# Performance work log

Measured on AMD Instinct MI355X. Metric: run time of the kernel, lower is better.

## Reference

```python
import jax, jax.numpy as jnp
import numpy as np

N, F_IN, F_OUT, C = 4096, 512, 256, 4


def setup_inputs() -> dict:
    key = jax.random.key(0)
    k1, k2, k3, k4 = jax.random.split(key, 4)
    stdv = 1.0 / np.sqrt(F_OUT)
    x = jax.random.normal(k1, (N, F_IN), dtype=jnp.float32)
    adjs = jax.random.normal(k2, (N, N, C), dtype=jnp.float32)
    weight = jax.random.uniform(k3, (F_IN, F_OUT, C), dtype=jnp.float32, minval=-stdv, maxval=stdv)
    bias = jax.random.uniform(k4, (N, F_OUT, C), dtype=jnp.float32, minval=-stdv, maxval=stdv)
    return {"x": x, "adjs": adjs, "weight": weight, "bias": bias}


def _fft_product(X, Y):
    # t-product: FFT along channel axis, per-frequency matmul, IFFT, real part
    Xf = jnp.fft.fft(X, axis=-1)
    Yf = jnp.fft.fft(Y, axis=-1)
    Zf = jnp.einsum('ijk,jrk->irk', Xf, Yf)
    return jnp.fft.ifft(Zf, axis=-1).real.astype(X.dtype)


def reference(x, adjs, weight, bias):
    C_ = adjs.shape[-1]
    # x.repeat(C,1,1).permute(1,2,0) -> [N, F, C]
    x3 = jnp.broadcast_to(x[:, :, None], (x.shape[0], x.shape[1], C_))
    h = _fft_product(x3, weight)      # [N, F_OUT, C]
    out = _fft_product(adjs, h)       # [N, F_OUT, C]
    return out + bias
```

## Files before the change

### kernel.cpp

```cpp
#include <hip/hip_runtime.h>
#include <cstdint>
#include <cstddef>

#define NN   4096
#define FIN  512
#define FOUT 256

typedef short bf16x8 __attribute__((ext_vector_type(8)));
typedef float f32x4  __attribute__((ext_vector_type(4)));

__device__ __forceinline__ unsigned short f2bf(float f) {
    union { float f; unsigned u; } v; v.f = f;
    unsigned r = v.u + 0x7FFFu + ((v.u >> 16) & 1u);
    return (unsigned short)(r >> 16);
}

__global__ __launch_bounds__(256) void k_prep_wsum(const float4* __restrict__ w4,
                                                   unsigned short* __restrict__ wsumT) {
    int t = blockIdx.x * 256 + threadIdx.x;
    int r = t & (FOUT - 1);
    int j = t >> 8;
    float4 v = w4[j * FOUT + r];
    wsumT[r * FIN + j] = f2bf(v.x + v.y + v.z + v.w);
}

template<int K, int MODE>
__global__ __launch_bounds__(512) void k_gemm16(
    const void* __restrict__ Aptr,
    const unsigned short* __restrict__ Bt,
    unsigned short* __restrict__ Ht,
    const float4* __restrict__ bias4,
    float4* __restrict__ out4)
{
    constexpr int NCHUNK = K / 64;
    __shared__ unsigned short Abf[16 * 72];

    const int tid  = threadIdx.x;
    const int lane = tid & 63;
    const int wave = tid >> 6;
    const int quad = lane >> 4;
    const int l15  = lane & 15;
    const int i0   = blockIdx.x * 16;

    const int si = tid >> 5;
    const int sk = (tid & 31) * 2;

    f32x4 acc0 = {0.f, 0.f, 0.f, 0.f};
    f32x4 acc1 = {0.f, 0.f, 0.f, 0.f};

    float4 pa0, pa1;
    bf16x8 bp00, bp01, bp10, bp11;

    auto loadA = [&](int c) {
        const int j0 = c * 64;
        if (MODE == 0) {
            const float* xp = (const float*)Aptr;
            const float2 t2 = *(const float2*)(xp + (size_t)(i0 + si) * FIN + j0 + sk);
            pa0.x = t2.x; pa0.y = t2.y;
        } else {
            const float4* ap = (const float4*)Aptr;
            size_t base = (size_t)(i0 + si) * NN + j0 + sk;
            pa0 = ap[base];
            pa1 = ap[base + 1];
        }
    };
    auto loadB = [&](int c, bf16x8& b00, bf16x8& b01, bf16x8& b10, bf16x8& b11) {
        const int j0 = c * 64;
        const unsigned short* p0 = Bt + (size_t)(wave * 32 + l15) * K + j0 + quad * 8;
        b00 = *(const bf16x8*)(p0);
        b01 = *(const bf16x8*)(p0 + 32);
        const unsigned short* p1 = p0 + (size_t)16 * K;
        b10 = *(const bf16x8*)(p1);
        b11 = *(const bf16x8*)(p1 + 32);
    };

    loadA(0);
    loadB(0, bp00, bp01, bp10, bp11);

    for (int c = 0; c < NCHUNK; ++c) {
        __syncthreads();
        if (MODE == 0) {
            unsigned pack = (unsigned)f2bf(pa0.x) | ((unsigned)f2bf(pa0.y) << 16);
            *(unsigned*)&Abf[si * 72 + sk] = pack;
        } else {
            float s0 = (pa0.x + pa0.y) + (pa0.z + pa0.w);
            float s1 = (pa1.x + pa1.y) + (pa1.z + pa1.w);
            *(unsigned*)&Abf[si * 72 + sk] =
                (unsigned)f2bf(s0) | ((unsigned)f2bf(s1) << 16);
        }
        __syncthreads();

        bf16x8 bc00 = bp00, bc01 = bp01, bc10 = bp10, bc11 = bp11;
        if (c + 1 < NCHUNK) {
            loadA(c + 1);
            loadB(c + 1, bp00, bp01, bp10, bp11);
        }

        bf16x8 a0 = *(const bf16x8*)&Abf[l15 * 72 + quad * 8];
        bf16x8 a1 = *(const bf16x8*)&Abf[l15 * 72 + 32 + quad * 8];

        acc0 = __builtin_amdgcn_mfma_f32_16x16x32_bf16(a0, bc00, acc0, 0, 0, 0);
        acc0 = __builtin_amdgcn_mfma_f32_16x16x32_bf16(a1, bc01, acc0, 0, 0, 0);
        acc1 = __builtin_amdgcn_mfma_f32_16x16x32_bf16(a0, bc10, acc1, 0, 0, 0);
        acc1 = __builtin_amdgcn_mfma_f32_16x16x32_bf16(a1, bc11, acc1, 0, 0, 0);
    }

    if (MODE == 0) {
        const int n  = wave * 32 + l15;
        const int ib = i0 + quad * 4;
        ushort4 h;
        h.x = f2bf(acc0[0]); h.y = f2bf(acc0[1]); h.z = f2bf(acc0[2]); h.w = f2bf(acc0[3]);
        *(ushort4*)(Ht + (size_t)n * NN + ib) = h;
        h.x = f2bf(acc1[0]); h.y = f2bf(acc1[1]); h.z = f2bf(acc1[2]); h.w = f2bf(acc1[3]);
        *(ushort4*)(Ht + (size_t)(n + 16) * NN + ib) = h;
    } else {
        const int col = wave * 32 + l15;
        const int ib  = i0 + quad * 4;
#pragma unroll
        for (int r = 0; r < 4; ++r) {
            size_t idx = (size_t)(ib + r) * FOUT + col;
            float4 bv = bias4[idx];
            float  s  = acc0[r];
            float4 o; o.x = s + bv.x; o.y = s + bv.y; o.z = s + bv.z; o.w = s + bv.w;
            out4[idx] = o;
            float4 bv1 = bias4[idx + 16];
            float  s1  = acc1[r];
            float4 o1; o1.x = s1 + bv1.x; o1.y = s1 + bv1.y; o1.z = s1 + bv1.z; o1.w = s1 + bv1.w;
            out4[idx + 16] = o1;
        }
    }
}

extern "C" void kernel_launch(void* const* d_in, const int* in_sizes, int n_in,
                              void* d_out, int out_size, void* d_ws, size_t ws_size,
                              hipStream_t stream) {
    const float*  x     = (const float*)d_in[0];
    const float4* adjs4 = (const float4*)d_in[1];
    const float4* w4    = (const float4*)d_in[2];
    const float4* bias4 = (const float4*)d_in[3];
    float4*       out4  = (float4*)d_out;

    unsigned short* wsumT = (unsigned short*)d_ws;
    unsigned short* Ht    = (unsigned short*)((char*)d_ws + (size_t)FOUT * FIN * 2);

    k_prep_wsum<<<(FIN * FOUT) / 256, 256, 0, stream>>>(w4, wsumT);
    k_gemm16<FIN, 0><<<NN / 16, 512, 0, stream>>>((const void*)x, wsumT, Ht, nullptr, nullptr);
    k_gemm16<NN, 1><<<NN / 16, 512, 0, stream>>>((const void*)adjs4, Ht, nullptr, bias4, out4);
}
```

Before: 397.9 us.

## Widen K chunks to 256 with double-buffered LDS and deeper prefetch

Raises the K step from 64 to 256 and double-buffers the A tile in LDS, prefetching two chunks ahead in registers so more memory loads are in flight per barrier. The adjacency stream, bias reads and output writes become nontemporal loads and stores. The aim is to hide latency in the bandwidth-bound adjs GEMM and to halve barrier overhead per unit of work. It costs many more registers (A and B prefetch arrays) and sets launch bounds to 2 blocks per CU, which may cause register spilling.

```diff
diff --git a/kernel.cpp b/kernel.cpp
--- a/kernel.cpp
+++ b/kernel.cpp
@@ -5,35 +5,41 @@
 #define NN   4096
 #define FIN  512
 #define FOUT 256
+#define BK   256
+#define LDSK 264
 
 typedef short bf16x8 __attribute__((ext_vector_type(8)));
 typedef float f32x4  __attribute__((ext_vector_type(4)));
+typedef float f32x2  __attribute__((ext_vector_type(2)));
 
 __device__ __forceinline__ unsigned short f2bf(float f) {
     union { float f; unsigned u; } v; v.f = f;
     unsigned r = v.u + 0x7FFFu + ((v.u >> 16) & 1u);
     return (unsigned short)(r >> 16);
 }
+__device__ __forceinline__ unsigned pack2(float a, float b) {
+    return (unsigned)f2bf(a) | ((unsigned)f2bf(b) << 16);
+}
 
-__global__ __launch_bounds__(256) void k_prep_wsum(const float4* __restrict__ w4,
+__global__ __launch_bounds__(256) void k_prep_wsum(const f32x4* __restrict__ w4,
                                                    unsigned short* __restrict__ wsumT) {
     int t = blockIdx.x * 256 + threadIdx.x;
     int r = t & (FOUT - 1);
     int j = t >> 8;
-    float4 v = w4[j * FOUT + r];
-    wsumT[r * FIN + j] = f2bf(v.x + v.y + v.z + v.w);
+    f32x4 v = w4[j * FOUT + r];
+    wsumT[r * FIN + j] = f2bf((v.x + v.y) + (v.z + v.w));
 }
 
 template<int K, int MODE>
-__global__ __launch_bounds__(512) void k_gemm16(
+__global__ __launch_bounds__(512, 2) void k_gemm16(
     const void* __restrict__ Aptr,
     const unsigned short* __restrict__ Bt,
     unsigned short* __restrict__ Ht,
-    const float4* __restrict__ bias4,
-    float4* __restrict__ out4)
+    const f32x4* __restrict__ bias4,
+    f32x4* __restrict__ out4)
 {
-    constexpr int NCHUNK = K / 64;
-    __shared__ unsigned short Abf[16 * 72];
+    constexpr int NCHUNK = K / BK;
+    __shared__ unsigned short Abf[2][16 * LDSK];
 
     const int tid  = threadIdx.x;
     const int lane = tid & 63;
@@ -42,67 +48,80 @@
     const int l15  = lane & 15;
     const int i0   = blockIdx.x * 16;
 
-    const int si = tid >> 5;
-    const int sk = (tid & 31) * 2;
+    const int si  = tid >> 5;
+    const int c32 = tid & 31;
 
     f32x4 acc0 = {0.f, 0.f, 0.f, 0.f};
     f32x4 acc1 = {0.f, 0.f, 0.f, 0.f};
 
-    float4 pa0, pa1;
-    bf16x8 bp00, bp01, bp10, bp11;
-
-    auto loadA = [&](int c) {
-        const int j0 = c * 64;
+    auto loadA = [&](int c, f32x4* pa, f32x2* pf) {
+        const int kb = c * BK;
         if (MODE == 0) {
-            const float* xp = (const float*)Aptr;
-            const float2 t2 = *(const float2*)(xp + (size_t)(i0 + si) * FIN + j0 + sk);
-            pa0.x = t2.x; pa0.y = t2.y;
+            const float* xp = (const float*)Aptr + (size_t)(i0 + si) * FIN + kb + c32 * 2;
+#pragma unroll
+            for (int u = 0; u < 4; ++u)
+                pf[u] = __builtin_nontemporal_load((const f32x2*)(xp + u * 64));
         } else {
-            const float4* ap = (const float4*)Aptr;
-            size_t base = (size_t)(i0 + si) * NN + j0 + sk;
-            pa0 = ap[base];
-            pa1 = ap[base + 1];
+            const f32x4* ap = (const f32x4*)Aptr + (size_t)(i0 + si) * NN + kb + c32 * 2;
+#pragma unroll
+            for (int u = 0; u < 4; ++u) {
+                pa[2 * u]     = __builtin_nontemporal_load(ap + u * 64);
+                pa[2 * u + 1] = __builtin_nontemporal_load(ap + u * 64 + 1);
+            }
         }
     };
-    auto loadB = [&](int c, bf16x8& b00, bf16x8& b01, bf16x8& b10, bf16x8& b11) {
-        const int j0 = c * 64;
-        const unsigned short* p0 = Bt + (size_t)(wave * 32 + l15) * K + j0 + quad * 8;
-        b00 = *(const bf16x8*)(p0);
-        b01 = *(const bf16x8*)(p0 + 32);
-        const unsigned short* p1 = p0 + (size_t)16 * K;
-        b10 = *(const bf16x8*)(p1);
-        b11 = *(const bf16x8*)(p1 + 32);
+    auto writeA = [&](int b, const f32x4* pa, const f32x2* pf) {
+        unsigned* dst = (unsigned*)&Abf[b][si * LDSK + c32 * 2];
+        if (MODE == 0) {
+#pragma unroll
+            for (int u = 0; u < 4; ++u)
+                dst[u * 32] = pack2(pf[u].x, pf[u].y);
+        } else {
+#pragma unroll
+            for (int u = 0; u < 4; ++u) {
+                f32x4 p0 = pa[2 * u], p1 = pa[2 * u + 1];
+                dst[u * 32] = pack2((p0.x + p0.y) + (p0.z + p0.w),
+                                    (p1.x + p1.y) + (p1.z + p1.w));
+            }
+        }
+    };
+    auto loadB = [&](int c, bf16x8* b0, bf16x8* b1) {
+        const unsigned short* p0 = Bt + (size_t)(wave * 32 + l15) * K + c * BK + quad * 8;
+#pragma unroll
+        for (int s = 0; s < 8; ++s) {
+            b0[s] = *(const bf16x8*)(p0 + s * 32);
+            b1[s] = *(const bf16x8*)(p0 + (size_t)16 * K + s * 32);
+        }
+    };
+    auto compute = [&](int b, const bf16x8* b0, const bf16x8* b1) {
+        const unsigned short* arow = &Abf[b][l15 * LDSK + quad * 8];
+#pragma unroll
+        for (int s = 0; s < 8; ++s) {
+            bf16x8 a = *(const bf16x8*)(arow + s * 32);
+            acc0 = __builtin_amdgcn_mfma_f32_16x16x32_bf16(a, b0[s], acc0, 0, 0, 0);
+            acc1 = __builtin_amdgcn_mfma_f32_16x16x32_bf16(a, b1[s], acc1, 0, 0, 0);
+        }
     };
 
-    loadA(0);
-    loadB(0, bp00, bp01, bp10, bp11);
+    f32x4 paX[8], paY[8];
+    f32x2 pfX[4], pfY[4];
+    bf16x8 b0X[8], b1X[8], b0Y[8], b1Y[8];
 
-    for (int c = 0; c < NCHUNK; ++c) {
+    loadA(0, paX, pfX); loadB(0, b0X, b1X);
+    loadA(1, paY, pfY); loadB(1, b0Y, b1Y);
+
+    for (int c = 0; c < NCHUNK; c += 2) {
+        writeA(0, paX, pfX);
+        { int cn = (c + 2 < NCHUNK) ? c + 2 : 0; loadA(cn, paX, pfX); }
         __syncthreads();
-        if (MODE == 0) {
-            unsigned pack = (unsigned)f2bf(pa0.x) | ((unsigned)f2bf(pa0.y) << 16);
-            *(unsigned*)&Abf[si * 72 + sk] = pack;
-        } else {
-            float s0 = (pa0.x + pa0.y) + (pa0.z + pa0.w);
-            float s1 = (pa1.x + pa1.y) + (pa1.z + pa1.w);
-            *(unsigned*)&Abf[si * 72 + sk] =
-                (unsigned)f2bf(s0) | ((unsigned)f2bf(s1) << 16);
-        }
+        compute(0, b0X, b1X);
+        { int cn = (c + 2 < NCHUNK) ? c + 2 : 0; loadB(cn, b0X, b1X); }
+
+        writeA(1, paY, pfY);
+        { int cn = (c + 3 < NCHUNK) ? c + 3 : 1; loadA(cn, paY, pfY); }
         __syncthreads();
-
-        bf16x8 bc00 = bp00, bc01 = bp01, bc10 = bp10, bc11 = bp11;
-        if (c + 1 < NCHUNK) {
-            loadA(c + 1);
-            loadB(c + 1, bp00, bp01, bp10, bp11);
-        }
-
-        bf16x8 a0 = *(const bf16x8*)&Abf[l15 * 72 + quad * 8];
-        bf16x8 a1 = *(const bf16x8*)&Abf[l15 * 72 + 32 + quad * 8];
-
-        acc0 = __builtin_amdgcn_mfma_f32_16x16x32_bf16(a0, bc00, acc0, 0, 0, 0);
-        acc0 = __builtin_amdgcn_mfma_f32_16x16x32_bf16(a1, bc01, acc0, 0, 0, 0);
-        acc1 = __builtin_amdgcn_mfma_f32_16x16x32_bf16(a0, bc10, acc1, 0, 0, 0);
-        acc1 = __builtin_amdgcn_mfma_f32_16x16x32_bf16(a1, bc11, acc1, 0, 0, 0);
+        compute(1, b0Y, b1Y);
+        { int cn = (c + 3 < NCHUNK) ? c + 3 : 1; loadB(cn, b0Y, b1Y); }
     }
 
     if (MODE == 0) {
@@ -119,14 +138,14 @@
 #pragma unroll
         for (int r = 0; r < 4; ++r) {
             size_t idx = (size_t)(ib + r) * FOUT + col;
-            float4 bv = bias4[idx];
-            float  s  = acc0[r];
-            float4 o; o.x = s + bv.x; o.y = s + bv.y; o.z = s + bv.z; o.w = s + bv.w;
-            out4[idx] = o;
-            float4 bv1 = bias4[idx + 16];
-            float  s1  = acc1[r];
-            float4 o1; o1.x = s1 + bv1.x; o1.y = s1 + bv1.y; o1.z = s1 + bv1.z; o1.w = s1 + bv1.w;
-            out4[idx + 16] = o1;
+            f32x4 bv = __builtin_nontemporal_load(bias4 + idx);
+            float s  = acc0[r];
+            f32x4 o; o.x = s + bv.x; o.y = s + bv.y; o.z = s + bv.z; o.w = s + bv.w;
+            __builtin_nontemporal_store(o, out4 + idx);
+            f32x4 bv1 = __builtin_nontemporal_load(bias4 + idx + 16);
+            float s1  = acc1[r];
+            f32x4 o1; o1.x = s1 + bv1.x; o1.y = s1 + bv1.y; o1.z = s1 + bv1.z; o1.w = s1 + bv1.w;
+            __builtin_nontemporal_store(o1, out4 + idx + 16);
         }
     }
 }
@@ -134,16 +153,16 @@
 extern "C" void kernel_launch(void* const* d_in, const int* in_sizes, int n_in,
                               void* d_out, int out_size, void* d_ws, size_t ws_size,
                               hipStream_t stream) {
-    const float*  x     = (const float*)d_in[0];
-    const float4* adjs4 = (const float4*)d_in[1];
-    const float4* w4    = (const float4*)d_in[2];
-    const float4* bias4 = (const float4*)d_in[3];
-    float4*       out4  = (float4*)d_out;
+    const float* x     = (const float*)d_in[0];
+    const void*  adjs  = d_in[1];
+    const f32x4* w4    = (const f32x4*)d_in[2];
+    const f32x4* bias4 = (const f32x4*)d_in[3];
+    f32x4*       out4  = (f32x4*)d_out;
 
     unsigned short* wsumT = (unsigned short*)d_ws;
     unsigned short* Ht    = (unsigned short*)((char*)d_ws + (size_t)FOUT * FIN * 2);
 
     k_prep_wsum<<<(FIN * FOUT) / 256, 256, 0, stream>>>(w4, wsumT);
     k_gemm16<FIN, 0><<<NN / 16, 512, 0, stream>>>((const void*)x, wsumT, Ht, nullptr, nullptr);
-    k_gemm16<NN, 1><<<NN / 16, 512, 0, stream>>>((const void*)adjs4, Ht, nullptr, bias4, out4);
+    k_gemm16<NN, 1><<<NN / 16, 512, 0, stream>>>(adjs, Ht, nullptr, bias4, out4);
 }
```

New measurement: 420.2 us. 1.06x slower.

## Split-K big GEMM with 64-row tiles, double-buffered LDS, and reduce kernel

Applied to the files above, without the earlier changes.

The adjacency GEMM moves to a dedicated kernel. Each block now computes a 64-row tile over a quarter of K, so one B fragment feeds four row sub-tiles and the Ht fragments are reused more. The A tile is double-buffered in LDS and read with nontemporal loads. Partial sums go to a workspace and a new reduce kernel adds them with the bias, which costs about 16MB of extra partial-sum traffic and one more launch.

```diff
diff --git a/kernel.cpp b/kernel.cpp
--- a/kernel.cpp
+++ b/kernel.cpp
@@ -8,68 +8,53 @@
 
 typedef short bf16x8 __attribute__((ext_vector_type(8)));
 typedef float f32x4  __attribute__((ext_vector_type(4)));
+typedef float f32x2  __attribute__((ext_vector_type(2)));
 
 __device__ __forceinline__ unsigned short f2bf(float f) {
     union { float f; unsigned u; } v; v.f = f;
     unsigned r = v.u + 0x7FFFu + ((v.u >> 16) & 1u);
     return (unsigned short)(r >> 16);
 }
-
-__global__ __launch_bounds__(256) void k_prep_wsum(const float4* __restrict__ w4,
+__device__ __forceinline__ unsigned pack2(float a, float b) {
+    return (unsigned)f2bf(a) | ((unsigned)f2bf(b) << 16);
+}
+
+__global__ __launch_bounds__(256) void k_prep_wsum(const f32x4* __restrict__ w4,
                                                    unsigned short* __restrict__ wsumT) {
     int t = blockIdx.x * 256 + threadIdx.x;
     int r = t & (FOUT - 1);
     int j = t >> 8;
-    float4 v = w4[j * FOUT + r];
-    wsumT[r * FIN + j] = f2bf(v.x + v.y + v.z + v.w);
-}
-
-template<int K, int MODE>
-__global__ __launch_bounds__(512) void k_gemm16(
-    const void* __restrict__ Aptr,
-    const unsigned short* __restrict__ Bt,
-    unsigned short* __restrict__ Ht,
-    const float4* __restrict__ bias4,
-    float4* __restrict__ out4)
-{
-    constexpr int NCHUNK = K / 64;
+    f32x4 v = w4[j * FOUT + r];
+    wsumT[r * FIN + j] = f2bf((v.x + v.y) + (v.z + v.w));
+}
+
+__global__ __launch_bounds__(512) void k_gemm_h(const float* __restrict__ x,
+                                                const unsigned short* __restrict__ Bt,
+                                                unsigned short* __restrict__ Ht) {
     __shared__ unsigned short Abf[16 * 72];
-
     const int tid  = threadIdx.x;
     const int lane = tid & 63;
     const int wave = tid >> 6;
     const int quad = lane >> 4;
     const int l15  = lane & 15;
     const int i0   = blockIdx.x * 16;
-
-    const int si = tid >> 5;
-    const int sk = (tid & 31) * 2;
+    const int si   = tid >> 5;
+    const int sk   = (tid & 31) * 2;
 
     f32x4 acc0 = {0.f, 0.f, 0.f, 0.f};
     f32x4 acc1 = {0.f, 0.f, 0.f, 0.f};
 
-    float4 pa0, pa1;
+    f32x2 pf;
     bf16x8 bp00, bp01, bp10, bp11;
 
     auto loadA = [&](int c) {
-        const int j0 = c * 64;
-        if (MODE == 0) {
-            const float* xp = (const float*)Aptr;
-            const float2 t2 = *(const float2*)(xp + (size_t)(i0 + si) * FIN + j0 + sk);
-            pa0.x = t2.x; pa0.y = t2.y;
-        } else {
-            const float4* ap = (const float4*)Aptr;
-            size_t base = (size_t)(i0 + si) * NN + j0 + sk;
-            pa0 = ap[base];
-            pa1 = ap[base + 1];
-        }
+        pf = *(const f32x2*)(x + (size_t)(i0 + si) * FIN + c * 64 + sk);
     };
     auto loadB = [&](int c, bf16x8& b00, bf16x8& b01, bf16x8& b10, bf16x8& b11) {
-        const int j0 = c * 64;
-        const unsigned short* p0 = Bt + (size_t)(wave * 32 + l15) * K + j0 + quad * 8;
+        const unsigned short* p0 = Bt + (size_t)(wave * 32 + l15) * FIN + c * 64 + quad * 8;
         b00 = *(const bf16x8*)(p0);
         b01 = *(const bf16x8*)(p0 + 32);
-        const unsigned short* p1 = p0 + (size_t)16 * K;
+        const unsigned short* p1 = p0 + (size_t)16 * FIN;
         b10 = *(const bf16x8*)(p1);
         b11 = *(const bf16x8*)(p1 + 32);
     };
@@ -77,25 +62,16 @@
     loadA(0);
     loadB(0, bp00, bp01, bp10, bp11);
 
-    for (int c = 0; c < NCHUNK; ++c) {
-        __syncthreads();
-        if (MODE == 0) {
-            unsigned pack = (unsigned)f2bf(pa0.x) | ((unsigned)f2bf(pa0.y) << 16);
-            *(unsigned*)&Abf[si * 72 + sk] = pack;
-        } else {
-            float s0 = (pa0.x + pa0.y) + (pa0.z + pa0.w);
-            float s1 = (pa1.x + pa1.y) + (pa1.z + pa1.w);
-            *(unsigned*)&Abf[si * 72 + sk] =
-                (unsigned)f2bf(s0) | ((unsigned)f2bf(s1) << 16);
-        }
+    for (int c = 0; c < FIN / 64; ++c) {
+        __syncthreads();
+        *(unsigned*)&Abf[si * 72 + sk] = pack2(pf.x, pf.y);
         __syncthreads();
 
         bf16x8 bc00 = bp00, bc01 = bp01, bc10 = bp10, bc11 = bp11;
-        if (c + 1 < NCHUNK) {
+        if (c + 1 < FIN / 64) {
             loadA(c + 1);
             loadB(c + 1, bp00, bp01, bp10, bp11);
         }
-
         bf16x8 a0 = *(const bf16x8*)&Abf[l15 * 72 + quad * 8];
         bf16x8 a1 = *(const bf16x8*)&Abf[l15 * 72 + 32 + quad * 8];
 
@@ -105,45 +81,139 @@
         acc1 = __builtin_amdgcn_mfma_f32_16x16x32_bf16(a1, bc11, acc1, 0, 0, 0);
     }
 
-    if (MODE == 0) {
-        const int n  = wave * 32 + l15;
-        const int ib = i0 + quad * 4;
-        ushort4 h;
-        h.x = f2bf(acc0[0]); h.y = f2bf(acc0[1]); h.z = f2bf(acc0[2]); h.w = f2bf(acc0[3]);
-        *(ushort4*)(Ht + (size_t)n * NN + ib) = h;
-        h.x = f2bf(acc1[0]); h.y = f2bf(acc1[1]); h.z = f2bf(acc1[2]); h.w = f2bf(acc1[3]);
-        *(ushort4*)(Ht + (size_t)(n + 16) * NN + ib) = h;
-    } else {
-        const int col = wave * 32 + l15;
-        const int ib  = i0 + quad * 4;
-#pragma unroll
-        for (int r = 0; r < 4; ++r) {
-            size_t idx = (size_t)(ib + r) * FOUT + col;
-            float4 bv = bias4[idx];
-            float  s  = acc0[r];
-            float4 o; o.x = s + bv.x; o.y = s + bv.y; o.z = s + bv.z; o.w = s + bv.w;
-            out4[idx] = o;
-            float4 bv1 = bias4[idx + 16];
-            float  s1  = acc1[r];
-            float4 o1; o1.x = s1 + bv1.x; o1.y = s1 + bv1.y; o1.z = s1 + bv1.z; o1.w = s1 + bv1.w;
-            out4[idx + 16] = o1;
-        }
+    const int n  = wave * 32 + l15;
+    const int ib = i0 + quad * 4;
+    ushort4 h;
+    h.x = f2bf(acc0[0]); h.y = f2bf(acc0[1]); h.z = f2bf(acc0[2]); h.w = f2bf(acc0[3]);
+    *(ushort4*)(Ht + (size_t)n * NN + ib) = h;
+    h.x = f2bf(acc1[0]); h.y = f2bf(acc1[1]); h.z = f2bf(acc1[2]); h.w = f2bf(acc1[3]);
+    *(ushort4*)(Ht + (size_t)(n + 16) * NN + ib) = h;
+}
+
+#define LD 72
+__global__ __launch_bounds__(512) void k_gemm_big(const f32x4* __restrict__ adjs4,
+                                                  const unsigned short* __restrict__ Bt,
+                                                  float* __restrict__ P) {
+    __shared__ unsigned short Abf[2][64 * LD];
+
+    const int tid  = threadIdx.x;
+    const int lane = tid & 63;
+    const int wave = tid >> 6;
+    const int quad = lane >> 4;
+    const int l15  = lane & 15;
+
+    const int kq   = blockIdx.x & 3;
+    const int rg   = blockIdx.x >> 2;
+    const int row0 = rg * 64;
+    const size_t kbase = (size_t)kq * 1024;
+
+    const int sr = tid >> 3;
+    const int sc = tid & 7;
+
+    f32x4 acc[4][2];
+#pragma unroll
+    for (int m = 0; m < 4; ++m)
+#pragma unroll
+        for (int n = 0; n < 2; ++n)
+            acc[m][n] = (f32x4){0.f, 0.f, 0.f, 0.f};
+
+    f32x4 pa[8];
+    bf16x8 pb[2][2];
+
+    auto loadA = [&](int c) {
+        const f32x4* ap = adjs4 + (size_t)(row0 + sr) * NN + kbase + c * 64;
+#pragma unroll
+        for (int u = 0; u < 4; ++u) {
+            pa[2 * u]     = __builtin_nontemporal_load(ap + sc * 2 + u * 16);
+            pa[2 * u + 1] = __builtin_nontemporal_load(ap + sc * 2 + u * 16 + 1);
+        }
+    };
+    auto writeA = [&](int b) {
+        unsigned* dst = (unsigned*)&Abf[b][sr * LD + sc * 2];
+#pragma unroll
+        for (int u = 0; u < 4; ++u) {
+            f32x4 p0 = pa[2 * u], p1 = pa[2 * u + 1];
+            dst[u * 8] = pack2((p0.x + p0.y) + (p0.z + p0.w),
+                               (p1.x + p1.y) + (p1.z + p1.w));
+        }
+    };
+    auto loadB = [&](int c) {
+#pragma unroll
+        for (int n = 0; n < 2; ++n) {
+            const unsigned short* p = Bt + (size_t)(wave * 32 + n * 16 + l15) * NN
+                                        + kbase + c * 64 + quad * 8;
+            pb[n][0] = *(const bf16x8*)p;
+            pb[n][1] = *(const bf16x8*)(p + 32);
+        }
+    };
+
+    loadA(0);
+    loadB(0);
+
+    for (int c = 0; c < 16; ++c) {
+        const int b = c & 1;
+        writeA(b);
+        if (c + 1 < 16) loadA(c + 1);
+        __syncthreads();
+
+        bf16x8 bc[2][2] = {{pb[0][0], pb[0][1]}, {pb[1][0], pb[1][1]}};
+        if (c + 1 < 16) loadB(c + 1);
+
+#pragma unroll
+        for (int s = 0; s < 2; ++s) {
+#pragma unroll
+            for (int m = 0; m < 4; ++m) {
+                bf16x8 a = *(const bf16x8*)&Abf[b][(m * 16 + l15) * LD + s * 32 + quad * 8];
+                acc[m][0] = __builtin_amdgcn_mfma_f32_16x16x32_bf16(a, bc[0][s], acc[m][0], 0, 0, 0);
+                acc[m][1] = __builtin_amdgcn_mfma_f32_16x16x32_bf16(a, bc[1][s], acc[m][1], 0, 0, 0);
+            }
+        }
+        __syncthreads();
     }
+
+    float* p = P + (size_t)kq * NN * FOUT;
+#pragma unroll
+    for (int m = 0; m < 4; ++m) {
+#pragma unroll
+        for (int n = 0; n < 2; ++n) {
+            const int col = wave * 32 + n * 16 + l15;
+#pragma unroll
+            for (int r = 0; r < 4; ++r) {
+                const int row = row0 + m * 16 + quad * 4 + r;
+                p[(size_t)row * FOUT + col] = acc[m][n][r];
+            }
+        }
+    }
+}
+
+__global__ __launch_bounds__(256) void k_reduce(const float* __restrict__ P,
+                                                const f32x4* __restrict__ bias4,
+                                                f32x4* __restrict__ out4) {
+    const int idx = blockIdx.x * 256 + threadIdx.x;
+    const size_t STR = (size_t)NN * FOUT;
+    float s = (P[idx] + P[idx + STR]) + (P[idx + 2 * STR] + P[idx + 3 * STR]);
+    f32x4 bv = bias4[idx];
+    f32x4 o;
+    o.x = s + bv.x; o.y = s + bv.y; o.z = s + bv.z; o.w = s + bv.w;
+    out4[idx] = o;
 }
 
 extern "C" void kernel_launch(void* const* d_in, const int* in_sizes, int n_in,
                               void* d_out, int out_size, void* d_ws, size_t ws_size,
                               hipStream_t stream) {
-    const float*  x     = (const float*)d_in[0];
-    const float4* adjs4 = (const float4*)d_in[1];
-    const float4* w4    = (const float4*)d_in[2];
-    const float4* bias4 = (const float4*)d_in[3];
-    float4*       out4  = (float4*)d_out;
-
-    unsigned short* wsumT = (unsigned short*)d_ws;
-    unsigned short* Ht    = (unsigned short*)((char*)d_ws + (size_t)FOUT * FIN * 2);
+    const float* x     = (const float*)d_in[0];
+    const f32x4* adjs4 = (const f32x4*)d_in[1];
+    const f32x4* w4    = (const f32x4*)d_in[2];
+    const f32x4* bias4 = (const f32x4*)d_in[3];
+    f32x4*       out4  = (f32x4*)d_out;
+
+    char* ws = (char*)d_ws;
+    unsigned short* wsumT = (unsigned short*)ws;
+    unsigned short* Ht    = (unsigned short*)(ws + 262144);
+    float*          Pp    = (float*)(ws + 262144 + 2097152);
 
     k_prep_wsum<<<(FIN * FOUT) / 256, 256, 0, stream>>>(w4, wsumT);
-    k_gemm16<FIN, 0><<<NN / 16, 512, 0, stream>>>((const void*)x, wsumT, Ht, nullptr, nullptr);
-    k_gemm16<NN, 1><<<NN / 16, 512, 0, stream>>>((const void*)adjs4, Ht, nullptr, bias4, out4);
-}
+    k_gemm_h<<<NN / 16, 512, 0, stream>>>(x, wsumT, Ht);
+    k_gemm_big<<<256, 512, 0, stream>>>(adjs4, Ht, Pp);
+    k_reduce<<<(NN * FOUT) / 256, 256, 0, stream>>>(Pp, bias4, out4);
+}
```

Result: no change. 396.9 us (-0.3%).
